# Performance work log

Hardware: AMD Instinct MI355X
Metric: run time of the kernel (lower is better)

The kernel has to match this reference:

```python
import jax, jax.numpy as jnp
import numpy as np
from jax import lax

BETA = 0.9   # membrane decay
THR = 1.0    # firing threshold (soft reset)
K = 10       # number of time bins
# spatial pyramid for original_shape=(100,368) under 4 stride-2 SAME convs
HW = [(50, 184), (25, 92), (13, 46), (7, 23)]
CH = [4, 8, 16, 32]


def conv(x, w, b, stride=1):
    y = lax.conv_general_dilated(x, w, (stride, stride), 'SAME',
                                 dimension_numbers=('NCHW', 'OIHW', 'NCHW'))
    return y + b[None, :, None, None]


def spike(u):
    # heaviside forward, sigmoid straight-through surrogate backward
    s = (u > 0.0).astype(u.dtype)
    sg = jax.nn.sigmoid(4.0 * u)
    return sg + lax.stop_gradient(s - sg)


def setup_inputs() -> dict:
    key = jax.random.key(0)
    ks = jax.random.split(key, 12)
    T, B = 1000, 1
    x = jax.random.normal(ks[0], (T, B, 1, 100, 368), jnp.float32)

    def w(k, o, i, kh=3, kw=3):
        return 0.1 * jax.random.normal(k, (o, i, kh, kw), jnp.float32)

    inp = {'x': x}
    cin = [1] + CH[:3]
    for li in range(4):
        inp['w%d' % (li + 1)] = w(ks[1 + li], CH[li], cin[li])
        inp['b%d' % (li + 1)] = jnp.zeros((CH[li],), jnp.float32)
    sc = [2 * K * c for c in CH]  # skip channels: [80,160,320,640]
    inp['dw4'] = w(ks[5], 64, sc[3]); inp['db4'] = jnp.zeros((64,), jnp.float32)
    inp['dw3'] = w(ks[6], 32, 64 + sc[2]); inp['db3'] = jnp.zeros((32,), jnp.float32)
    inp['dw2'] = w(ks[7], 16, 32 + sc[1]); inp['db2'] = jnp.zeros((16,), jnp.float32)
    inp['dw1'] = w(ks[8], 8, 16 + sc[0]); inp['db1'] = jnp.zeros((8,), jnp.float32)
    inp['wo'] = w(ks[9], 1, 8, 1, 1); inp['bo'] = jnp.zeros((1,), jnp.float32)
    inp['total_steps'] = 1000
    inp['block_size'] = 100
    return inp


def reference(x, w1, b1, w2, b2, w3, b3, w4, b4,
              dw4, db4, dw3, db3, dw2, db2, dw1, db1, wo, bo,
              total_steps, block_size):
    S = total_steps // K  # steps per bin
    B = x.shape[1]
    xb = x.reshape((K, S) + x.shape[1:])  # [K,S,B,C,H,W]
    mems0 = tuple(jnp.zeros((B, CH[i], HW[i][0], HW[i][1]), x.dtype) for i in range(4))
    enc_w = [(w1, b1), (w2, b2), (w3, b3), (w4, b4)]

    def forward_step(x_t, mems):
        new_mems, spk = [], x_t
        for (wi, bi), m in zip(enc_w, mems):
            m = BETA * m + conv(spk, wi, bi, 2)
            spk = spike(m - THR)
            m = m - spk * THR  # soft reset
            new_mems.append(m)
        return tuple(new_mems)

    def step(carry, x_t):
        mems, sums, sqs = carry
        mems = forward_step(x_t, mems)
        sums = tuple(s + m for s, m in zip(sums, mems))
        sqs = tuple(q + m * m for q, m in zip(sqs, mems))
        return (mems, sums, sqs), None

    def bin_fn(mems, x_bin):
        zeros = tuple(jnp.zeros_like(m) for m in mems)
        (mems, sums, sqs), _ = lax.scan(step, (mems, zeros, zeros), x_bin)
        means = tuple(s / S for s in sums)
        stds = tuple(jnp.sqrt(jnp.maximum(q / S - mu * mu, 1e-8))
                     for q, mu in zip(sqs, means))
        return mems, (means, stds)

    _, (means, stds) = lax.scan(bin_fn, mems0, xb)  # each leaf: [K,B,C,H,W]

    def skip(mean, std):
        # torch.cat([mean0,std0,mean1,std1,...], dim=1) channel ordering
        f = jnp.stack([mean, std], axis=1)        # [K,2,B,C,H,W]
        f = jnp.transpose(f, (2, 0, 1, 3, 4, 5))  # [B,K,2,C,H,W]
        b_, k_, t_, c_, h_, w_ = f.shape
        return f.reshape(b_, k_ * t_ * c_, h_, w_)

    skips = [skip(means[i], stds[i]) for i in range(4)]

    def up(t, hw):
        return jax.image.resize(t, (t.shape[0], t.shape[1], hw[0], hw[1]), 'bilinear')

    relu = jax.nn.relu
    d = relu(conv(skips[3], dw4, db4))
    d = relu(conv(jnp.concatenate([up(d, HW[2]), skips[2]], 1), dw3, db3))
    d = relu(conv(jnp.concatenate([up(d, HW[1]), skips[1]], 1), dw2, db2))
    d = relu(conv(jnp.concatenate([up(d, HW[0]), skips[0]], 1), dw1, db1))
    tau_c = conv(up(d, (100, 368)), wo, bo)  # [B,1,100,368]
    return tau_c
```

## Files before the change

### kernel.cpp

```cpp
#include <hip/hip_runtime.h>

#define KBINS  10
#define SBIN   100
#define BETA   0.9f
#define THR    1.0f
#define CDIV(a,b) (((a)+(b)-1)/(b))


__global__ void k_zero16(float4* __restrict__ p, int n16) {
    int i = blockIdx.x * blockDim.x + threadIdx.x;
    if (i < n16) p[i] = make_float4(0.f, 0.f, 0.f, 0.f);
}

__global__ void k_conv1(const float* __restrict__ x,
                        const float* __restrict__ w1,
                        const float* __restrict__ b1,
                        float* __restrict__ c1, int tcount) {
    int n = blockIdx.x * blockDim.x + threadIdx.x;
    if (n >= tcount * 50 * 46) return;
    int wq  = n % 46;
    int tmp = n / 46;
    int h   = tmp % 50;
    int t   = tmp / 50;
    int w0  = wq * 4;

    const float* xt = x + (size_t)t * 36800;
    float rm2 = (h  < 49)  ? 1.f : 0.f;
    float cm8 = (w0 < 180) ? 1.f : 0.f;
    int   r2  = min(2 * h + 2, 99);
    int   cb  = 2 * w0;
    int   c8  = min(cb + 8, 367);

    const float* row0 = xt + (2 * h) * 368 + cb;
    const float* row1 = row0 + 368;
    const float* row2 = xt + r2 * 368 + cb;

    float tap[3][9];
    #pragma unroll
    for (int j = 0; j < 8; j++) {
        tap[0][j] = row0[j];
        tap[1][j] = row1[j];
        tap[2][j] = row2[j] * rm2;
    }
    tap[0][8] = xt[(2 * h) * 368 + c8] * cm8;
    tap[1][8] = xt[(2 * h + 1) * 368 + c8] * cm8;
    tap[2][8] = xt[r2 * 368 + c8] * (rm2 * cm8);

    float* ot = c1 + (size_t)t * 36800 + h * 184 + w0;
    #pragma unroll
    for (int co = 0; co < 4; co++) {
        float b = b1[co];
        float a0 = b, a1 = b, a2 = b, a3 = b;
        #pragma unroll
        for (int r = 0; r < 3; r++) {
            #pragma unroll
            for (int kw = 0; kw < 3; kw++) {
                float wv = w1[co * 9 + r * 3 + kw];
                a0 = fmaf(tap[r][0 + kw], wv, a0);
                a1 = fmaf(tap[r][2 + kw], wv, a1);
                a2 = fmaf(tap[r][4 + kw], wv, a2);
                a3 = fmaf(tap[r][6 + kw], wv, a3);
            }
        }
        *(float4*)(ot + (size_t)co * 9200) = make_float4(a0, a1, a2, a3);
    }
}

__global__ void k_scan(const float* __restrict__ cbuf,
                       unsigned char* __restrict__ spk,
                       float* __restrict__ skip,
                       float* __restrict__ mstate,
                       int C, int HW, int Win, int Wp, int HpWp,
                       int write_spk, int bin0, int nbins, int init) {
    const int PF = 20;
    int CHW = C * HW;
    int p = blockIdx.x * blockDim.x + threadIdx.x;
    if (p >= CHW) return;
    int c  = p / HW;
    int hw = p - c * HW;
    int h  = hw / Win, w = hw - h * Win;

    const size_t tstr = (size_t)C * HpWp;
    unsigned char* sp = spk + (size_t)bin0 * SBIN * tstr
                      + (size_t)c * HpWp + (h + 1) * Wp + (w + 1);

    float m = init ? 0.0f : mstate[p];
    float va[PF], vb[PF];
    #pragma unroll
    for (int j = 0; j < PF; j++) va[j] = cbuf[(size_t)j * CHW + p];

    const int T = nbins * SBIN;
    for (int k = 0; k < nbins; k++) {
        float s = 0.0f, q = 0.0f;
        for (int b = 0; b < SBIN / PF; b++) {
            int t0 = k * SBIN + b * PF;
            int tn = t0 + PF;
            bool more = (tn < T);
            #pragma unroll
            for (int j = 0; j < PF; j++)
                vb[j] = more ? cbuf[(size_t)(tn + j) * CHW + p] : 0.0f;
            #pragma unroll
            for (int j = 0; j < PF; j++) {
                m = fmaf(m, BETA, va[j]);
                float spv = (m - THR > 0.0f) ? 1.0f : 0.0f;
                m -= spv * THR;
                if (write_spk) sp[(size_t)(t0 + j) * tstr] = (unsigned char)spv;
                s += m;
                q = fmaf(m, m, q);
            }
            #pragma unroll
            for (int j = 0; j < PF; j++) va[j] = vb[j];
        }
        int g = bin0 + k;
        float mean = s * (1.0f / SBIN);
        float var  = q * (1.0f / SBIN) - mean * mean;
        float sd   = sqrtf(fmaxf(var, 1e-8f));
        skip[(size_t)(g * 2 * C + c) * HW + hw]     = mean;
        skip[(size_t)(g * 2 * C + C + c) * HW + hw] = sd;
    }
    mstate[p] = m;
}

template<int CIN, int COUT, int COG, int OW,
         int HOUT, int WOUT, int PADH, int HP, int WP>
__global__ void k_convs2(const unsigned char* __restrict__ spk,
                         const float* __restrict__ wt,
                         const float* __restrict__ bias,
                         float* __restrict__ out) {
    const int WQ = (WOUT + OW - 1) / OW;
    const int NT = 2 * OW + 1;
    int n = blockIdx.x * blockDim.x + threadIdx.x;
    if (n >= 1000 * HOUT * WQ) return;
    int wq  = n % WQ;
    int tmp = n / WQ;
    int h   = tmp % HOUT;
    int t   = tmp / HOUT;
    int cog = blockIdx.y;
    int w0  = wq * OW;

    const unsigned char* base = spk + (size_t)t * CIN * HP * WP
                              + (2 * h - PADH + 1) * WP + (2 * w0 + 1);

    float acc[OW][COG];
    #pragma unroll
    for (int q = 0; q < OW; q++)
        #pragma unroll
        for (int co = 0; co < COG; co++) acc[q][co] = bias[cog * COG + co];

    for (int ci = 0; ci < CIN; ci++) {
        const unsigned char* ic = base + (size_t)ci * HP * WP;
        float tap[3][NT];
        #pragma unroll
        for (int r = 0; r < 3; r++)
            #pragma unroll
            for (int j = 0; j < NT; j++)
                tap[r][j] = (float)ic[r * WP + j];
        #pragma unroll
        for (int co = 0; co < COG; co++) {
            const float* wc = wt + ((size_t)(cog * COG + co) * CIN + ci) * 9;
            #pragma unroll
            for (int r = 0; r < 3; r++)
                #pragma unroll
                for (int kw = 0; kw < 3; kw++) {
                    float wv = wc[r * 3 + kw];
                    #pragma unroll
                    for (int q = 0; q < OW; q++)
                        acc[q][co] = fmaf(tap[r][2 * q + kw], wv, acc[q][co]);
                }
        }
    }

    float* ot = out + ((size_t)t * COUT + cog * COG) * (HOUT * WOUT) + h * WOUT + w0;
    #pragma unroll
    for (int co = 0; co < COG; co++) {
        float* oc = ot + (size_t)co * (HOUT * WOUT);
        if constexpr (OW == 4) {
            *(float4*)oc = make_float4(acc[0][co], acc[1][co], acc[2][co], acc[3][co]);
        } else {
            if (w0 + 2 <= WOUT) *(float2*)oc = make_float2(acc[0][co], acc[1][co]);
            else                oc[0] = acc[0][co];
        }
    }
}

__global__ void k_up_cat(const float* __restrict__ up_src, int Cup, int Hi, int Wi,
                         const float* __restrict__ skip, int Cskip,
                         float* __restrict__ out, int Ho, int Wo) {
    int total = (Cup + Cskip) * Ho * Wo;
    int n = blockIdx.x * blockDim.x + threadIdx.x;
    if (n >= total) return;
    int w   = n % Wo;
    int tmp = n / Wo;
    int h   = tmp % Ho;
    int c   = tmp / Ho;
    float v;
    if (c < Cup) {
        float ph = (h + 0.5f) * (float)Hi / (float)Ho - 0.5f;
        float pw = (w + 0.5f) * (float)Wi / (float)Wo - 0.5f;
        float fh = floorf(ph), fw = floorf(pw);
        int h0 = (int)fh, w0 = (int)fw;
        float ah = ph - fh, aw = pw - fw;
        int h0c = min(max(h0, 0), Hi - 1), h1c = min(max(h0 + 1, 0), Hi - 1);
        int w0c = min(max(w0, 0), Wi - 1), w1c = min(max(w0 + 1, 0), Wi - 1);
        const float* sc = up_src + (size_t)c * Hi * Wi;
        float v00 = sc[h0c * Wi + w0c], v01 = sc[h0c * Wi + w1c];
        float v10 = sc[h1c * Wi + w0c], v11 = sc[h1c * Wi + w1c];
        v = (1.0f - ah) * ((1.0f - aw) * v00 + aw * v01)
          + ah * ((1.0f - aw) * v10 + aw * v11);
    } else {
        v = skip[(size_t)(c - Cup) * Ho * Wo + h * Wo + w];
    }
    out[n] = v;
}

template<int CIN, int CS, int COG>
__global__ void k_dconv(const float* __restrict__ in,
                        const float* __restrict__ wt,
                        float* __restrict__ part,
                        int Cout, int H, int W) {
    int HW  = H * W;
    int pix = blockIdx.x * blockDim.x + threadIdx.x;
    if (pix >= HW) return;
    int co0   = blockIdx.y * COG;
    int chunk = blockIdx.z;
    int h = pix / W, w = pix - h * W;

    int off[9]; float msk[9];
    #pragma unroll
    for (int kh = 0; kh < 3; kh++) {
        int r = h + kh - 1;
        bool rok = (r >= 0) && (r < H);
        int rc = rok ? r : 0;
        #pragma unroll
        for (int kw = 0; kw < 3; kw++) {
            int cc = w + kw - 1;
            bool cok = (cc >= 0) && (cc < W);
            int ccc = cok ? cc : 0;
            off[kh * 3 + kw] = rc * W + ccc;
            msk[kh * 3 + kw] = (rok && cok) ? 1.0f : 0.0f;
        }
    }

    const float* ibase = in + (size_t)chunk * CS * HW;
    const float* wbase = wt + ((size_t)co0 * CIN + (size_t)chunk * CS) * 9;

    float acc[COG];
    #pragma unroll
    for (int co = 0; co < COG; co++) acc[co] = 0.0f;

    #pragma unroll 8
    for (int ci = 0; ci < CS; ci++) {
        const float* ic = ibase + (size_t)ci * HW;
        float tap[9];
        #pragma unroll
        for (int j = 0; j < 9; j++)
            tap[j] = msk[j] * ic[off[j]];
        #pragma unroll
        for (int co = 0; co < COG; co++) {
            const float* wc = wbase + ((size_t)co * CIN + ci) * 9;
            #pragma unroll
            for (int j = 0; j < 9; j++)
                acc[co] = fmaf(tap[j], wc[j], acc[co]);
        }
    }

    float* pp = part + ((size_t)chunk * Cout + co0) * HW + pix;
    #pragma unroll
    for (int co = 0; co < COG; co++) pp[(size_t)co * HW] = acc[co];
}

__global__ void k_reduce_relu(const float* __restrict__ part,
                              const float* __restrict__ bias,
                              float* __restrict__ out,
                              int Cout, int HW, int nchunks) {
    int n = blockIdx.x * blockDim.x + threadIdx.x;
    if (n >= Cout * HW) return;
    int co = n / HW;
    float acc = bias[co];
    for (int c = 0; c < nchunks; c++)
        acc += part[(size_t)c * Cout * HW + n];
    out[n] = fmaxf(acc, 0.0f);
}

__global__ void k_final(const float* __restrict__ d1,
                        const float* __restrict__ wo,
                        const float* __restrict__ bo,
                        float* __restrict__ out) {
    int n = blockIdx.x * blockDim.x + threadIdx.x;
    if (n >= 36800) return;
    int w = n % 368, h = n / 368;
    float ph = (h + 0.5f) * 0.5f - 0.5f;
    float pw = (w + 0.5f) * 0.5f - 0.5f;
    float fh = floorf(ph), fw = floorf(pw);
    int h0 = (int)fh, w0 = (int)fw;
    float ah = ph - fh, aw = pw - fw;
    int h0c = min(max(h0, 0), 49),  h1c = min(max(h0 + 1, 0), 49);
    int w0c = min(max(w0, 0), 183), w1c = min(max(w0 + 1, 0), 183);
    float acc = bo[0];
    #pragma unroll
    for (int c = 0; c < 8; c++) {
        const float* sc = d1 + c * 9200;
        float v00 = sc[h0c * 184 + w0c], v01 = sc[h0c * 184 + w1c];
        float v10 = sc[h1c * 184 + w0c], v11 = sc[h1c * 184 + w1c];
        float v = (1.0f - ah) * ((1.0f - aw) * v00 + aw * v01)
                + ah * ((1.0f - aw) * v10 + aw * v11);
        acc = fmaf(wo[c], v, acc);
    }
    out[n] = acc;
}

extern "C" void kernel_launch(void* const* d_in, const int* in_sizes, int n_in,
                              void* d_out, int out_size, void* d_ws, size_t ws_size,
                              hipStream_t stream) {
    (void)in_sizes; (void)n_in; (void)out_size; (void)ws_size;
    const float* x   = (const float*)d_in[0];
    const float* w1  = (const float*)d_in[1];
    const float* b1  = (const float*)d_in[2];
    const float* w2  = (const float*)d_in[3];
    const float* b2  = (const float*)d_in[4];
    const float* w3  = (const float*)d_in[5];
    const float* b3  = (const float*)d_in[6];
    const float* w4  = (const float*)d_in[7];
    const float* b4  = (const float*)d_in[8];
    const float* dw4 = (const float*)d_in[9];
    const float* db4 = (const float*)d_in[10];
    const float* dw3 = (const float*)d_in[11];
    const float* db3 = (const float*)d_in[12];
    const float* dw2 = (const float*)d_in[13];
    const float* db2 = (const float*)d_in[14];
    const float* dw1 = (const float*)d_in[15];
    const float* db1 = (const float*)d_in[16];
    const float* wo  = (const float*)d_in[17];
    const float* bo  = (const float*)d_in[18];
    float* out = (float*)d_out;

    char* ws = (char*)d_ws;
    size_t off = 0;
    auto alloc = [&](size_t bytes) -> void* {
        void* p = ws + off;
        off += (bytes + 255) & ~(size_t)255;
        return p;
    };
    float* cbuf = (float*)alloc(73600000);
    unsigned char* spk1r = (unsigned char*)alloc(39936000 + 256);
    unsigned char* spk2r = (unsigned char*)alloc(21600000 + 256);
    unsigned char* spk3r = (unsigned char*)alloc(12960000 + 256);
    unsigned char* spk1p = spk1r + 63;
    unsigned char* spk2p = spk2r + 63;
    unsigned char* spk3p = spk3r + 63;
    float* skip0 = (float*)alloc(2944000);
    float* skip1 = (float*)alloc(1472000);
    float* skip2 = (float*)alloc(765440);
    float* skip3 = (float*)alloc(412160);
    float* msS   = (float*)alloc(147200);
    char* dec = (char*)cbuf;
    size_t doff = 0;
    auto dalloc = [&](size_t bytes) -> void* {
        void* p = dec + doff;
        doff += (bytes + 255) & ~(size_t)255;
        return p;
    };
    float* d4   = (float*)dalloc(10304u * 4);
    float* d3   = (float*)dalloc(19136u * 4);
    float* d2   = (float*)dalloc(36800u * 4);
    float* d1   = (float*)dalloc(73600u * 4);
    float* cat3 = (float*)dalloc(229632u * 4);
    float* cat2 = (float*)dalloc(441600u * 4);
    float* cat1 = (float*)dalloc(883200u * 4);
    float* part = (float*)dalloc(230400u * 4);

    const int BS  = 256;
    const int SBS = 64;

    {
        size_t nb = (39936000 + 256) + (21600000 + 256) + (12960000 + 256);
        int n16 = (int)(nb / 16);
        k_zero16<<<CDIV(n16, BS), BS, 0, stream>>>((float4*)spk1r, n16);
    }

    for (int q = 0; q < 2; q++) {
        k_conv1<<<CDIV(500 * 50 * 46, BS), BS, 0, stream>>>(
            x + (size_t)q * 500 * 36800, w1, b1, cbuf, 500);
        k_scan<<<CDIV(36800, SBS), SBS, 0, stream>>>(
            cbuf, spk1p, skip0, msS, 4, 9200, 184, 192, 52 * 192,
            1, 5 * q, 5, (q == 0) ? 1 : 0);
    }

    k_convs2<4, 8, 8, 4, 25, 92, 0, 52, 192>
        <<<dim3(CDIV(1000 * 25 * 23, BS), 1), BS, 0, stream>>>(spk1p, w2, b2, cbuf);
    k_scan<<<CDIV(18400, SBS), SBS, 0, stream>>>(cbuf, spk2p, skip1, msS,
                                                 8, 2300, 92, 100, 27 * 100, 1, 0, 10, 1);

    k_convs2<8, 16, 16, 2, 13, 46, 1, 27, 100>
        <<<dim3(CDIV(1000 * 13 * 23, BS), 1), BS, 0, stream>>>(spk2p, w3, b3, cbuf);
    k_scan<<<CDIV(9568, SBS), SBS, 0, stream>>>(cbuf, spk3p, skip2, msS,
                                                16, 598, 46, 54, 15 * 54, 1, 0, 10, 1);

    k_convs2<16, 32, 16, 2, 7, 23, 1, 15, 54>
        <<<dim3(CDIV(1000 * 7 * 12, BS), 2), BS, 0, stream>>>(spk3p, w4, b4, cbuf);
    k_scan<<<CDIV(5152, SBS), SBS, 0, stream>>>(cbuf, spk1p , skip3, msS,
                                                32, 161, 23, 31, 9 * 31, 0, 0, 10, 1);

    {
        dim3 g(CDIV(161, 64), 16, 20);
        k_dconv<640, 32, 4><<<g, 64, 0, stream>>>(skip3, dw4, part, 64, 7, 23);
        k_reduce_relu<<<CDIV(64 * 161, BS), BS, 0, stream>>>(part, db4, d4, 64, 161, 20);
    }
    {
        k_up_cat<<<CDIV(384 * 598, BS), BS, 0, stream>>>(d4, 64, 7, 23,
                                                         skip2, 320, cat3, 13, 46);
        dim3 g(CDIV(598, 64), 8, 12);
        k_dconv<384, 32, 4><<<g, 64, 0, stream>>>(cat3, dw3, part, 32, 13, 46);
        k_reduce_relu<<<CDIV(32 * 598, BS), BS, 0, stream>>>(part, db3, d3, 32, 598, 12);
    }
    {
        k_up_cat<<<CDIV(192 * 2300, BS), BS, 0, stream>>>(d3, 32, 13, 46,
                                                          skip1, 160, cat2, 25, 92);
        dim3 g(CDIV(2300, 128), 4, 6);
        k_dconv<192, 32, 4><<<g, 128, 0, stream>>>(cat2, dw2, part, 16, 25, 92);
        k_reduce_relu<<<CDIV(16 * 2300, BS), BS, 0, stream>>>(part, db2, d2, 16, 2300, 6);
    }
    {
        k_up_cat<<<CDIV(96 * 9200, BS), BS, 0, stream>>>(d2, 16, 25, 92,
                                                         skip0, 80, cat1, 50, 184);
        dim3 g(CDIV(9200, BS), 2, 3);
        k_dconv<96, 32, 4><<<g, BS, 0, stream>>>(cat1, dw1, part, 8, 50, 184);
        k_reduce_relu<<<CDIV(8 * 9200, BS), BS, 0, stream>>>(part, db1, d1, 8, 9200, 3);
    }
    k_final<<<CDIV(36800, BS), BS, 0, stream>>>(d1, wo, bo, out);
}
```

Measured before the change: 837.3 us.

## Fuse all stages into one cooperative persistent kernel with grid syncs

Turns every stage (zeroing, conv1, scans, stride-2 convs, decoder convs, reductions, upsample-concat, final) into a device function run by one cooperative kernel with grid-stride loops and grid-wide barriers between stages. The aim is to remove the cost of launching about 25 separate kernels. In exchange, the grid is capped at 256 or 512 blocks, which limits parallelism in the big stages. The scan stages also expose only a few thousand threads, and the grid-wide syncs add their own overhead. A fallback multi-kernel path is kept for when the cooperative launch fails.

```diff
diff --git a/kernel.cpp b/kernel.cpp
--- a/kernel.cpp
+++ b/kernel.cpp
@@ -1,4 +1,7 @@
 #include <hip/hip_runtime.h>
+#include <hip/hip_cooperative_groups.h>
+
+namespace cg = cooperative_groups;
 
 #define KBINS  10
 #define SBIN   100
@@ -7,332 +10,446 @@
 #define CDIV(a,b) (((a)+(b)-1)/(b))
 
 
-__global__ void k_zero16(float4* __restrict__ p, int n16) {
-    int i = blockIdx.x * blockDim.x + threadIdx.x;
-    if (i < n16) p[i] = make_float4(0.f, 0.f, 0.f, 0.f);
-}
-
-__global__ void k_conv1(const float* __restrict__ x,
-                        const float* __restrict__ w1,
-                        const float* __restrict__ b1,
-                        float* __restrict__ c1, int tcount) {
-    int n = blockIdx.x * blockDim.x + threadIdx.x;
-    if (n >= tcount * 50 * 46) return;
-    int wq  = n % 46;
-    int tmp = n / 46;
-    int h   = tmp % 50;
-    int t   = tmp / 50;
-    int w0  = wq * 4;
-
-    const float* xt = x + (size_t)t * 36800;
-    float rm2 = (h  < 49)  ? 1.f : 0.f;
-    float cm8 = (w0 < 180) ? 1.f : 0.f;
-    int   r2  = min(2 * h + 2, 99);
-    int   cb  = 2 * w0;
-    int   c8  = min(cb + 8, 367);
-
-    const float* row0 = xt + (2 * h) * 368 + cb;
-    const float* row1 = row0 + 368;
-    const float* row2 = xt + r2 * 368 + cb;
-
-    float tap[3][9];
-    #pragma unroll
-    for (int j = 0; j < 8; j++) {
-        tap[0][j] = row0[j];
-        tap[1][j] = row1[j];
-        tap[2][j] = row2[j] * rm2;
-    }
-    tap[0][8] = xt[(2 * h) * 368 + c8] * cm8;
-    tap[1][8] = xt[(2 * h + 1) * 368 + c8] * cm8;
-    tap[2][8] = xt[r2 * 368 + c8] * (rm2 * cm8);
-
-    float* ot = c1 + (size_t)t * 36800 + h * 184 + w0;
-    #pragma unroll
-    for (int co = 0; co < 4; co++) {
-        float b = b1[co];
-        float a0 = b, a1 = b, a2 = b, a3 = b;
-        #pragma unroll
-        for (int r = 0; r < 3; r++) {
-            #pragma unroll
-            for (int kw = 0; kw < 3; kw++) {
-                float wv = w1[co * 9 + r * 3 + kw];
-                a0 = fmaf(tap[r][0 + kw], wv, a0);
-                a1 = fmaf(tap[r][2 + kw], wv, a1);
-                a2 = fmaf(tap[r][4 + kw], wv, a2);
-                a3 = fmaf(tap[r][6 + kw], wv, a3);
+struct MegaParams {
+    const float *x, *w1, *b1, *w2, *b2, *w3, *b3, *w4, *b4;
+    const float *dw4, *db4, *dw3, *db3, *dw2, *db2, *dw1, *db1, *wo, *bo;
+    float* out;
+    float* cbuf;
+    unsigned char *spk1r;
+    unsigned char *spk1p, *spk2p, *spk3p;
+    float *skip0, *skip1, *skip2, *skip3, *msS;
+    float *d4, *d3, *d2, *d1, *cat3, *cat2, *cat1, *part;
+};
+
+
+__device__ inline void st_zero(unsigned char* base, int n16, int tid, int NT) {
+    float4* z = (float4*)base;
+    for (int i = tid; i < n16; i += NT)
+        z[i] = make_float4(0.f, 0.f, 0.f, 0.f);
+}
+
+__device__ inline void st_conv1(const float* x, const float* w1, const float* b1,
+                                float* cbuf, int q, int tid, int NT) {
+    const int N = 500 * 50 * 46;
+    const float* xb = x + (size_t)q * 500 * 36800;
+    for (int n = tid; n < N; n += NT) {
+        int wq  = n % 46;
+        int tmp = n / 46;
+        int h   = tmp % 50;
+        int t   = tmp / 50;
+        int w0  = wq * 4;
+
+        const float* xt = xb + (size_t)t * 36800;
+        float rm2 = (h  < 49)  ? 1.f : 0.f;
+        float cm8 = (w0 < 180) ? 1.f : 0.f;
+        int   r2  = min(2 * h + 2, 99);
+        int   cb  = 2 * w0;
+        int   c8  = min(cb + 8, 367);
+
+        const float* row0 = xt + (2 * h) * 368 + cb;
+        const float* row1 = row0 + 368;
+        const float* row2 = xt + r2 * 368 + cb;
+
+        float tap[3][9];
+        #pragma unroll
+        for (int j = 0; j < 8; j++) {
+            tap[0][j] = row0[j];
+            tap[1][j] = row1[j];
+            tap[2][j] = row2[j] * rm2;
+        }
+        tap[0][8] = xt[(2 * h) * 368 + c8] * cm8;
+        tap[1][8] = xt[(2 * h + 1) * 368 + c8] * cm8;
+        tap[2][8] = xt[r2 * 368 + c8] * (rm2 * cm8);
+
+        float* ot = cbuf + (size_t)t * 36800 + h * 184 + w0;
+        #pragma unroll
+        for (int co = 0; co < 4; co++) {
+            float b = b1[co];
+            float a0 = b, a1 = b, a2 = b, a3 = b;
+            #pragma unroll
+            for (int r = 0; r < 3; r++) {
+                #pragma unroll
+                for (int kw = 0; kw < 3; kw++) {
+                    float wv = w1[co * 9 + r * 3 + kw];
+                    a0 = fmaf(tap[r][0 + kw], wv, a0);
+                    a1 = fmaf(tap[r][2 + kw], wv, a1);
+                    a2 = fmaf(tap[r][4 + kw], wv, a2);
+                    a3 = fmaf(tap[r][6 + kw], wv, a3);
+                }
             }
-        }
-        *(float4*)(ot + (size_t)co * 9200) = make_float4(a0, a1, a2, a3);
-    }
-}
-
-__global__ void k_scan(const float* __restrict__ cbuf,
-                       unsigned char* __restrict__ spk,
-                       float* __restrict__ skip,
-                       float* __restrict__ mstate,
-                       int C, int HW, int Win, int Wp, int HpWp,
-                       int write_spk, int bin0, int nbins, int init) {
+            *(float4*)(ot + (size_t)co * 9200) = make_float4(a0, a1, a2, a3);
+        }
+    }
+}
+
+__device__ inline void st_scan(const float* cbuf, unsigned char* spk,
+                               float* skip, float* mstate,
+                               int C, int HW, int Win, int Wp, int HpWp,
+                               int write_spk, int bin0, int nbins, int init,
+                               int tid, int NT) {
     const int PF = 20;
     int CHW = C * HW;
-    int p = blockIdx.x * blockDim.x + threadIdx.x;
-    if (p >= CHW) return;
-    int c  = p / HW;
-    int hw = p - c * HW;
-    int h  = hw / Win, w = hw - h * Win;
-
-    const size_t tstr = (size_t)C * HpWp;
-    unsigned char* sp = spk + (size_t)bin0 * SBIN * tstr
-                      + (size_t)c * HpWp + (h + 1) * Wp + (w + 1);
-
-    float m = init ? 0.0f : mstate[p];
-    float va[PF], vb[PF];
-    #pragma unroll
-    for (int j = 0; j < PF; j++) va[j] = cbuf[(size_t)j * CHW + p];
-
-    const int T = nbins * SBIN;
-    for (int k = 0; k < nbins; k++) {
-        float s = 0.0f, q = 0.0f;
-        for (int b = 0; b < SBIN / PF; b++) {
-            int t0 = k * SBIN + b * PF;
-            int tn = t0 + PF;
-            bool more = (tn < T);
-            #pragma unroll
-            for (int j = 0; j < PF; j++)
-                vb[j] = more ? cbuf[(size_t)(tn + j) * CHW + p] : 0.0f;
-            #pragma unroll
-            for (int j = 0; j < PF; j++) {
-                m = fmaf(m, BETA, va[j]);
-                float spv = (m - THR > 0.0f) ? 1.0f : 0.0f;
-                m -= spv * THR;
-                if (write_spk) sp[(size_t)(t0 + j) * tstr] = (unsigned char)spv;
-                s += m;
-                q = fmaf(m, m, q);
+    for (int p = tid; p < CHW; p += NT) {
+        int c  = p / HW;
+        int hw = p - c * HW;
+        int h  = hw / Win, w = hw - h * Win;
+
+        const size_t tstr = (size_t)C * HpWp;
+        unsigned char* sp = spk + (size_t)bin0 * SBIN * tstr
+                          + (size_t)c * HpWp + (h + 1) * Wp + (w + 1);
+
+        float m = init ? 0.0f : mstate[p];
+        float va[PF], vb[PF];
+        #pragma unroll
+        for (int j = 0; j < PF; j++) va[j] = cbuf[(size_t)j * CHW + p];
+
+        const int T = nbins * SBIN;
+        for (int k = 0; k < nbins; k++) {
+            float s = 0.0f, q = 0.0f;
+            for (int b = 0; b < SBIN / PF; b++) {
+                int t0 = k * SBIN + b * PF;
+                int tn = t0 + PF;
+                bool more = (tn < T);
+                #pragma unroll
+                for (int j = 0; j < PF; j++)
+                    vb[j] = more ? cbuf[(size_t)(tn + j) * CHW + p] : 0.0f;
+                #pragma unroll
+                for (int j = 0; j < PF; j++) {
+                    m = fmaf(m, BETA, va[j]);
+                    float spv = (m - THR > 0.0f) ? 1.0f : 0.0f;
+                    m -= spv * THR;
+                    if (write_spk) sp[(size_t)(t0 + j) * tstr] = (unsigned char)spv;
+                    s += m;
+                    q = fmaf(m, m, q);
+                }
+                #pragma unroll
+                for (int j = 0; j < PF; j++) va[j] = vb[j];
             }
-            #pragma unroll
-            for (int j = 0; j < PF; j++) va[j] = vb[j];
-        }
-        int g = bin0 + k;
-        float mean = s * (1.0f / SBIN);
-        float var  = q * (1.0f / SBIN) - mean * mean;
-        float sd   = sqrtf(fmaxf(var, 1e-8f));
-        skip[(size_t)(g * 2 * C + c) * HW + hw]     = mean;
-        skip[(size_t)(g * 2 * C + C + c) * HW + hw] = sd;
-    }
-    mstate[p] = m;
+            int g = bin0 + k;
+            float mean = s * (1.0f / SBIN);
+            float var  = q * (1.0f / SBIN) - mean * mean;
+            float sd   = sqrtf(fmaxf(var, 1e-8f));
+            skip[(size_t)(g * 2 * C + c) * HW + hw]     = mean;
+            skip[(size_t)(g * 2 * C + C + c) * HW + hw] = sd;
+        }
+        mstate[p] = m;
+    }
 }
 
 template<int CIN, int COUT, int COG, int OW,
-         int HOUT, int WOUT, int PADH, int HP, int WP>
-__global__ void k_convs2(const unsigned char* __restrict__ spk,
-                         const float* __restrict__ wt,
-                         const float* __restrict__ bias,
-                         float* __restrict__ out) {
-    const int WQ = (WOUT + OW - 1) / OW;
-    const int NT = 2 * OW + 1;
-    int n = blockIdx.x * blockDim.x + threadIdx.x;
-    if (n >= 1000 * HOUT * WQ) return;
-    int wq  = n % WQ;
-    int tmp = n / WQ;
-    int h   = tmp % HOUT;
-    int t   = tmp / HOUT;
-    int cog = blockIdx.y;
-    int w0  = wq * OW;
-
-    const unsigned char* base = spk + (size_t)t * CIN * HP * WP
-                              + (2 * h - PADH + 1) * WP + (2 * w0 + 1);
-
-    float acc[OW][COG];
-    #pragma unroll
-    for (int q = 0; q < OW; q++)
-        #pragma unroll
-        for (int co = 0; co < COG; co++) acc[q][co] = bias[cog * COG + co];
-
-    for (int ci = 0; ci < CIN; ci++) {
-        const unsigned char* ic = base + (size_t)ci * HP * WP;
-        float tap[3][NT];
-        #pragma unroll
-        for (int r = 0; r < 3; r++)
-            #pragma unroll
-            for (int j = 0; j < NT; j++)
-                tap[r][j] = (float)ic[r * WP + j];
-        #pragma unroll
-        for (int co = 0; co < COG; co++) {
-            const float* wc = wt + ((size_t)(cog * COG + co) * CIN + ci) * 9;
+         int HOUT, int WOUT, int PADH, int HP, int WP, int NCOG>
+__device__ inline void st_convs2(const unsigned char* spk, const float* wt,
+                                 const float* bias, float* out,
+                                 int tid, int NT) {
+    const int WQ  = (WOUT + OW - 1) / OW;
+    const int NB  = 1000 * HOUT * WQ;
+    const int NBr = (NB + 63) & ~63;
+    const int NT9 = 2 * OW + 1;
+    for (int i = tid; i < NBr * NCOG; i += NT) {
+        int cog = i / NBr;
+        int n   = i - cog * NBr;
+        bool ok = (n < NB);
+        n = ok ? n : 0;
+        int wq  = n % WQ;
+        int tmp = n / WQ;
+        int h   = tmp % HOUT;
+        int t   = tmp / HOUT;
+        int w0  = wq * OW;
+
+        const unsigned char* base = spk + (size_t)t * CIN * HP * WP
+                                  + (2 * h - PADH + 1) * WP + (2 * w0 + 1);
+
+        float acc[OW][COG];
+        #pragma unroll
+        for (int q = 0; q < OW; q++)
+            #pragma unroll
+            for (int co = 0; co < COG; co++) acc[q][co] = bias[cog * COG + co];
+
+        for (int ci = 0; ci < CIN; ci++) {
+            const unsigned char* ic = base + (size_t)ci * HP * WP;
+            float tap[3][NT9];
             #pragma unroll
             for (int r = 0; r < 3; r++)
                 #pragma unroll
-                for (int kw = 0; kw < 3; kw++) {
-                    float wv = wc[r * 3 + kw];
+                for (int j = 0; j < NT9; j++)
+                    tap[r][j] = (float)ic[r * WP + j];
+            #pragma unroll
+            for (int co = 0; co < COG; co++) {
+                const float* wc = wt + ((size_t)(cog * COG + co) * CIN + ci) * 9;
+                #pragma unroll
+                for (int r = 0; r < 3; r++)
                     #pragma unroll
-                    for (int q = 0; q < OW; q++)
-                        acc[q][co] = fmaf(tap[r][2 * q + kw], wv, acc[q][co]);
+                    for (int kw = 0; kw < 3; kw++) {
+                        float wv = wc[r * 3 + kw];
+                        #pragma unroll
+                        for (int q = 0; q < OW; q++)
+                            acc[q][co] = fmaf(tap[r][2 * q + kw], wv, acc[q][co]);
+                    }
+            }
+        }
+
+        if (ok) {
+            float* ot = out + ((size_t)t * COUT + cog * COG) * (HOUT * WOUT)
+                      + h * WOUT + w0;
+            #pragma unroll
+            for (int co = 0; co < COG; co++) {
+                float* oc = ot + (size_t)co * (HOUT * WOUT);
+                if constexpr (OW == 4) {
+                    *(float4*)oc = make_float4(acc[0][co], acc[1][co],
+                                               acc[2][co], acc[3][co]);
+                } else {
+                    if (w0 + 2 <= WOUT) *(float2*)oc = make_float2(acc[0][co], acc[1][co]);
+                    else                oc[0] = acc[0][co];
                 }
-        }
-    }
-
-    float* ot = out + ((size_t)t * COUT + cog * COG) * (HOUT * WOUT) + h * WOUT + w0;
-    #pragma unroll
-    for (int co = 0; co < COG; co++) {
-        float* oc = ot + (size_t)co * (HOUT * WOUT);
-        if constexpr (OW == 4) {
-            *(float4*)oc = make_float4(acc[0][co], acc[1][co], acc[2][co], acc[3][co]);
+            }
+        }
+    }
+}
+
+__device__ inline void st_upcat(const float* up_src, int Cup, int Hi, int Wi,
+                                const float* skip, int Cskip,
+                                float* out, int Ho, int Wo, int tid, int NT) {
+    int total = (Cup + Cskip) * Ho * Wo;
+    for (int n = tid; n < total; n += NT) {
+        int w   = n % Wo;
+        int tmp = n / Wo;
+        int h   = tmp % Ho;
+        int c   = tmp / Ho;
+        float v;
+        if (c < Cup) {
+            float ph = (h + 0.5f) * (float)Hi / (float)Ho - 0.5f;
+            float pw = (w + 0.5f) * (float)Wi / (float)Wo - 0.5f;
+            float fh = floorf(ph), fw = floorf(pw);
+            int h0 = (int)fh, w0 = (int)fw;
+            float ah = ph - fh, aw = pw - fw;
+            int h0c = min(max(h0, 0), Hi - 1), h1c = min(max(h0 + 1, 0), Hi - 1);
+            int w0c = min(max(w0, 0), Wi - 1), w1c = min(max(w0 + 1, 0), Wi - 1);
+            const float* sc = up_src + (size_t)c * Hi * Wi;
+            float v00 = sc[h0c * Wi + w0c], v01 = sc[h0c * Wi + w1c];
+            float v10 = sc[h1c * Wi + w0c], v11 = sc[h1c * Wi + w1c];
+            v = (1.0f - ah) * ((1.0f - aw) * v00 + aw * v01)
+              + ah * ((1.0f - aw) * v10 + aw * v11);
         } else {
-            if (w0 + 2 <= WOUT) *(float2*)oc = make_float2(acc[0][co], acc[1][co]);
-            else                oc[0] = acc[0][co];
-        }
-    }
-}
-
-__global__ void k_up_cat(const float* __restrict__ up_src, int Cup, int Hi, int Wi,
-                         const float* __restrict__ skip, int Cskip,
-                         float* __restrict__ out, int Ho, int Wo) {
-    int total = (Cup + Cskip) * Ho * Wo;
-    int n = blockIdx.x * blockDim.x + threadIdx.x;
-    if (n >= total) return;
-    int w   = n % Wo;
-    int tmp = n / Wo;
-    int h   = tmp % Ho;
-    int c   = tmp / Ho;
-    float v;
-    if (c < Cup) {
-        float ph = (h + 0.5f) * (float)Hi / (float)Ho - 0.5f;
-        float pw = (w + 0.5f) * (float)Wi / (float)Wo - 0.5f;
+            v = skip[(size_t)(c - Cup) * Ho * Wo + h * Wo + w];
+        }
+        out[n] = v;
+    }
+}
+
+template<int CIN, int CS, int COG>
+__device__ inline void st_dconv(const float* in, const float* wt, float* part,
+                                int Cout, int H, int W, int nchunks,
+                                int tid, int NT) {
+    int HW  = H * W;
+    int HWr = (HW + 63) & ~63;
+    int ncog = Cout / COG;
+    int total = nchunks * ncog * HWr;
+    for (int i = tid; i < total; i += NT) {
+        int pix = i % HWr;
+        int r   = i / HWr;
+        int co0   = (r % ncog) * COG;
+        int chunk = r / ncog;
+        bool ok = (pix < HW);
+        pix = ok ? pix : 0;
+        int h = pix / W, w = pix - h * W;
+
+        int off[9]; float msk[9];
+        #pragma unroll
+        for (int kh = 0; kh < 3; kh++) {
+            int rr = h + kh - 1;
+            bool rok = (rr >= 0) && (rr < H);
+            int rc = rok ? rr : 0;
+            #pragma unroll
+            for (int kw = 0; kw < 3; kw++) {
+                int cc = w + kw - 1;
+                bool cok = (cc >= 0) && (cc < W);
+                int ccc = cok ? cc : 0;
+                off[kh * 3 + kw] = rc * W + ccc;
+                msk[kh * 3 + kw] = (rok && cok) ? 1.0f : 0.0f;
+            }
+        }
+
+        const float* ibase = in + (size_t)chunk * CS * HW;
+        const float* wbase = wt + ((size_t)co0 * CIN + (size_t)chunk * CS) * 9;
+
+        float acc[COG];
+        #pragma unroll
+        for (int co = 0; co < COG; co++) acc[co] = 0.0f;
+
+        #pragma unroll 8
+        for (int ci = 0; ci < CS; ci++) {
+            const float* ic = ibase + (size_t)ci * HW;
+            float tap[9];
+            #pragma unroll
+            for (int j = 0; j < 9; j++)
+                tap[j] = msk[j] * ic[off[j]];
+            #pragma unroll
+            for (int co = 0; co < COG; co++) {
+                const float* wc = wbase + ((size_t)co * CIN + ci) * 9;
+                #pragma unroll
+                for (int j = 0; j < 9; j++)
+                    acc[co] = fmaf(tap[j], wc[j], acc[co]);
+            }
+        }
+
+        if (ok) {
+            float* pp = part + ((size_t)chunk * Cout + co0) * HW + pix;
+            #pragma unroll
+            for (int co = 0; co < COG; co++) pp[(size_t)co * HW] = acc[co];
+        }
+    }
+}
+
+__device__ inline void st_reduce(const float* part, const float* bias,
+                                 float* out, int Cout, int HW, int nchunks,
+                                 int tid, int NT) {
+    int total = Cout * HW;
+    for (int n = tid; n < total; n += NT) {
+        int co = n / HW;
+        float acc = bias[co];
+        for (int c = 0; c < nchunks; c++)
+            acc += part[(size_t)c * Cout * HW + n];
+        out[n] = fmaxf(acc, 0.0f);
+    }
+}
+
+__device__ inline void st_final(const float* d1, const float* wo,
+                                const float* bo, float* out, int tid, int NT) {
+    for (int n = tid; n < 36800; n += NT) {
+        int w = n % 368, h = n / 368;
+        float ph = (h + 0.5f) * 0.5f - 0.5f;
+        float pw = (w + 0.5f) * 0.5f - 0.5f;
         float fh = floorf(ph), fw = floorf(pw);
         int h0 = (int)fh, w0 = (int)fw;
         float ah = ph - fh, aw = pw - fw;
-        int h0c = min(max(h0, 0), Hi - 1), h1c = min(max(h0 + 1, 0), Hi - 1);
-        int w0c = min(max(w0, 0), Wi - 1), w1c = min(max(w0 + 1, 0), Wi - 1);
-        const float* sc = up_src + (size_t)c * Hi * Wi;
-        float v00 = sc[h0c * Wi + w0c], v01 = sc[h0c * Wi + w1c];
-        float v10 = sc[h1c * Wi + w0c], v11 = sc[h1c * Wi + w1c];
-        v = (1.0f - ah) * ((1.0f - aw) * v00 + aw * v01)
-          + ah * ((1.0f - aw) * v10 + aw * v11);
-    } else {
-        v = skip[(size_t)(c - Cup) * Ho * Wo + h * Wo + w];
-    }
-    out[n] = v;
-}
-
+        int h0c = min(max(h0, 0), 49),  h1c = min(max(h0 + 1, 0), 49);
+        int w0c = min(max(w0, 0), 183), w1c = min(max(w0 + 1, 0), 183);
+        float acc = bo[0];
+        #pragma unroll
+        for (int c = 0; c < 8; c++) {
+            const float* sc = d1 + c * 9200;
+            float v00 = sc[h0c * 184 + w0c], v01 = sc[h0c * 184 + w1c];
+            float v10 = sc[h1c * 184 + w0c], v11 = sc[h1c * 184 + w1c];
+            float v = (1.0f - ah) * ((1.0f - aw) * v00 + aw * v01)
+                    + ah * ((1.0f - aw) * v10 + aw * v11);
+            acc = fmaf(wo[c], v, acc);
+        }
+        out[n] = acc;
+    }
+}
+
+__global__ void __launch_bounds__(256, 2) k_mega(MegaParams P) {
+    cg::grid_group grid = cg::this_grid();
+    const int tid = blockIdx.x * 256 + threadIdx.x;
+    const int NT  = gridDim.x * 256;
+
+    st_zero(P.spk1r, 74496768 / 16, tid, NT);
+    grid.sync();
+
+    for (int q = 0; q < 2; q++) {
+        st_conv1(P.x, P.w1, P.b1, P.cbuf, q, tid, NT);
+        grid.sync();
+        st_scan(P.cbuf, P.spk1p, P.skip0, P.msS, 4, 9200, 184, 192, 9984,
+                1, 5 * q, 5, (q == 0) ? 1 : 0, tid, NT);
+        grid.sync();
+    }
+
+    st_convs2<4, 8, 8, 4, 25, 92, 0, 52, 192, 1>(P.spk1p, P.w2, P.b2, P.cbuf, tid, NT);
+    grid.sync();
+    st_scan(P.cbuf, P.spk2p, P.skip1, P.msS, 8, 2300, 92, 100, 2700,
+            1, 0, 10, 1, tid, NT);
+    grid.sync();
+
+    st_convs2<8, 16, 16, 2, 13, 46, 1, 27, 100, 1>(P.spk2p, P.w3, P.b3, P.cbuf, tid, NT);
+    grid.sync();
+    st_scan(P.cbuf, P.spk3p, P.skip2, P.msS, 16, 598, 46, 54, 810,
+            1, 0, 10, 1, tid, NT);
+    grid.sync();
+
+    st_convs2<16, 32, 16, 2, 7, 23, 1, 15, 54, 2>(P.spk3p, P.w4, P.b4, P.cbuf, tid, NT);
+    grid.sync();
+    st_scan(P.cbuf, P.spk1p , P.skip3, P.msS, 32, 161, 23, 31, 279,
+            0, 0, 10, 1, tid, NT);
+    grid.sync();
+
+    st_dconv<640, 32, 4>(P.skip3, P.dw4, P.part, 64, 7, 23, 20, tid, NT);
+    grid.sync();
+    st_reduce(P.part, P.db4, P.d4, 64, 161, 20, tid, NT);
+    grid.sync();
+    st_upcat(P.d4, 64, 7, 23, P.skip2, 320, P.cat3, 13, 46, tid, NT);
+    grid.sync();
+    st_dconv<384, 32, 4>(P.cat3, P.dw3, P.part, 32, 13, 46, 12, tid, NT);
+    grid.sync();
+    st_reduce(P.part, P.db3, P.d3, 32, 598, 12, tid, NT);
+    grid.sync();
+    st_upcat(P.d3, 32, 13, 46, P.skip1, 160, P.cat2, 25, 92, tid, NT);
+    grid.sync();
+    st_dconv<192, 32, 4>(P.cat2, P.dw2, P.part, 16, 25, 92, 6, tid, NT);
+    grid.sync();
+    st_reduce(P.part, P.db2, P.d2, 16, 2300, 6, tid, NT);
+    grid.sync();
+    st_upcat(P.d2, 16, 25, 92, P.skip0, 80, P.cat1, 50, 184, tid, NT);
+    grid.sync();
+    st_dconv<96, 32, 4>(P.cat1, P.dw1, P.part, 8, 50, 184, 3, tid, NT);
+    grid.sync();
+    st_reduce(P.part, P.db1, P.d1, 8, 9200, 3, tid, NT);
+    grid.sync();
+
+    st_final(P.d1, P.wo, P.bo, P.out, tid, NT);
+}
+
+#define TIDNT int tid = blockIdx.x * blockDim.x + threadIdx.x; \
+              int NT = gridDim.x * blockDim.x;
+
+__global__ void g_zero(unsigned char* base, int n16) { TIDNT; st_zero(base, n16, tid, NT); }
+__global__ void g_conv1(const float* x, const float* w1, const float* b1,
+                        float* cbuf, int q) { TIDNT; st_conv1(x, w1, b1, cbuf, q, tid, NT); }
+__global__ void g_scan(const float* cbuf, unsigned char* spk, float* skip,
+                       float* mstate, int C, int HW, int Win, int Wp, int HpWp,
+                       int write_spk, int bin0, int nbins, int init) {
+    TIDNT; st_scan(cbuf, spk, skip, mstate, C, HW, Win, Wp, HpWp,
+                   write_spk, bin0, nbins, init, tid, NT);
+}
+template<int CIN, int COUT, int COG, int OW,
+         int HOUT, int WOUT, int PADH, int HP, int WP, int NCOG>
+__global__ void g_convs2(const unsigned char* spk, const float* wt,
+                         const float* bias, float* out) {
+    TIDNT; st_convs2<CIN, COUT, COG, OW, HOUT, WOUT, PADH, HP, WP, NCOG>(
+        spk, wt, bias, out, tid, NT);
+}
+__global__ void g_upcat(const float* u, int Cup, int Hi, int Wi,
+                        const float* s, int Cs, float* o, int Ho, int Wo) {
+    TIDNT; st_upcat(u, Cup, Hi, Wi, s, Cs, o, Ho, Wo, tid, NT);
+}
 template<int CIN, int CS, int COG>
-__global__ void k_dconv(const float* __restrict__ in,
-                        const float* __restrict__ wt,
-                        float* __restrict__ part,
-                        int Cout, int H, int W) {
-    int HW  = H * W;
-    int pix = blockIdx.x * blockDim.x + threadIdx.x;
-    if (pix >= HW) return;
-    int co0   = blockIdx.y * COG;
-    int chunk = blockIdx.z;
-    int h = pix / W, w = pix - h * W;
-
-    int off[9]; float msk[9];
-    #pragma unroll
-    for (int kh = 0; kh < 3; kh++) {
-        int r = h + kh - 1;
-        bool rok = (r >= 0) && (r < H);
-        int rc = rok ? r : 0;
-        #pragma unroll
-        for (int kw = 0; kw < 3; kw++) {
-            int cc = w + kw - 1;
-            bool cok = (cc >= 0) && (cc < W);
-            int ccc = cok ? cc : 0;
-            off[kh * 3 + kw] = rc * W + ccc;
-            msk[kh * 3 + kw] = (rok && cok) ? 1.0f : 0.0f;
-        }
-    }
-
-    const float* ibase = in + (size_t)chunk * CS * HW;
-    const float* wbase = wt + ((size_t)co0 * CIN + (size_t)chunk * CS) * 9;
-
-    float acc[COG];
-    #pragma unroll
-    for (int co = 0; co < COG; co++) acc[co] = 0.0f;
-
-    #pragma unroll 8
-    for (int ci = 0; ci < CS; ci++) {
-        const float* ic = ibase + (size_t)ci * HW;
-        float tap[9];
-        #pragma unroll
-        for (int j = 0; j < 9; j++)
-            tap[j] = msk[j] * ic[off[j]];
-        #pragma unroll
-        for (int co = 0; co < COG; co++) {
-            const float* wc = wbase + ((size_t)co * CIN + ci) * 9;
-            #pragma unroll
-            for (int j = 0; j < 9; j++)
-                acc[co] = fmaf(tap[j], wc[j], acc[co]);
-        }
-    }
-
-    float* pp = part + ((size_t)chunk * Cout + co0) * HW + pix;
-    #pragma unroll
-    for (int co = 0; co < COG; co++) pp[(size_t)co * HW] = acc[co];
-}
-
-__global__ void k_reduce_relu(const float* __restrict__ part,
-                              const float* __restrict__ bias,
-                              float* __restrict__ out,
-                              int Cout, int HW, int nchunks) {
-    int n = blockIdx.x * blockDim.x + threadIdx.x;
-    if (n >= Cout * HW) return;
-    int co = n / HW;
-    float acc = bias[co];
-    for (int c = 0; c < nchunks; c++)
-        acc += part[(size_t)c * Cout * HW + n];
-    out[n] = fmaxf(acc, 0.0f);
-}
-
-__global__ void k_final(const float* __restrict__ d1,
-                        const float* __restrict__ wo,
-                        const float* __restrict__ bo,
-                        float* __restrict__ out) {
-    int n = blockIdx.x * blockDim.x + threadIdx.x;
-    if (n >= 36800) return;
-    int w = n % 368, h = n / 368;
-    float ph = (h + 0.5f) * 0.5f - 0.5f;
-    float pw = (w + 0.5f) * 0.5f - 0.5f;
-    float fh = floorf(ph), fw = floorf(pw);
-    int h0 = (int)fh, w0 = (int)fw;
-    float ah = ph - fh, aw = pw - fw;
-    int h0c = min(max(h0, 0), 49),  h1c = min(max(h0 + 1, 0), 49);
-    int w0c = min(max(w0, 0), 183), w1c = min(max(w0 + 1, 0), 183);
-    float acc = bo[0];
-    #pragma unroll
-    for (int c = 0; c < 8; c++) {
-        const float* sc = d1 + c * 9200;
-        float v00 = sc[h0c * 184 + w0c], v01 = sc[h0c * 184 + w1c];
-        float v10 = sc[h1c * 184 + w0c], v11 = sc[h1c * 184 + w1c];
-        float v = (1.0f - ah) * ((1.0f - aw) * v00 + aw * v01)
-                + ah * ((1.0f - aw) * v10 + aw * v11);
-        acc = fmaf(wo[c], v, acc);
-    }
-    out[n] = acc;
-}
+__global__ void g_dconv(const float* in, const float* wt, float* part,
+                        int Cout, int H, int W, int nchunks) {
+    TIDNT; st_dconv<CIN, CS, COG>(in, wt, part, Cout, H, W, nchunks, tid, NT);
+}
+__global__ void g_reduce(const float* part, const float* bias, float* out,
+                         int Cout, int HW, int nchunks) {
+    TIDNT; st_reduce(part, bias, out, Cout, HW, nchunks, tid, NT);
+}
+__global__ void g_final(const float* d1, const float* wo, const float* bo,
+                        float* out) { TIDNT; st_final(d1, wo, bo, out, tid, NT); }
 
 extern "C" void kernel_launch(void* const* d_in, const int* in_sizes, int n_in,
                               void* d_out, int out_size, void* d_ws, size_t ws_size,
                               hipStream_t stream) {
     (void)in_sizes; (void)n_in; (void)out_size; (void)ws_size;
-    const float* x   = (const float*)d_in[0];
-    const float* w1  = (const float*)d_in[1];
-    const float* b1  = (const float*)d_in[2];
-    const float* w2  = (const float*)d_in[3];
-    const float* b2  = (const float*)d_in[4];
-    const float* w3  = (const float*)d_in[5];
-    const float* b3  = (const float*)d_in[6];
-    const float* w4  = (const float*)d_in[7];
-    const float* b4  = (const float*)d_in[8];
-    const float* dw4 = (const float*)d_in[9];
-    const float* db4 = (const float*)d_in[10];
-    const float* dw3 = (const float*)d_in[11];
-    const float* db3 = (const float*)d_in[12];
-    const float* dw2 = (const float*)d_in[13];
-    const float* db2 = (const float*)d_in[14];
-    const float* dw1 = (const float*)d_in[15];
-    const float* db1 = (const float*)d_in[16];
-    const float* wo  = (const float*)d_in[17];
-    const float* bo  = (const float*)d_in[18];
-    float* out = (float*)d_out;
+
+    MegaParams P;
+    P.x   = (const float*)d_in[0];
+    P.w1  = (const float*)d_in[1];  P.b1 = (const float*)d_in[2];
+    P.w2  = (const float*)d_in[3];  P.b2 = (const float*)d_in[4];
+    P.w3  = (const float*)d_in[5];  P.b3 = (const float*)d_in[6];
+    P.w4  = (const float*)d_in[7];  P.b4 = (const float*)d_in[8];
+    P.dw4 = (const float*)d_in[9];  P.db4 = (const float*)d_in[10];
+    P.dw3 = (const float*)d_in[11]; P.db3 = (const float*)d_in[12];
+    P.dw2 = (const float*)d_in[13]; P.db2 = (const float*)d_in[14];
+    P.dw1 = (const float*)d_in[15]; P.db1 = (const float*)d_in[16];
+    P.wo  = (const float*)d_in[17]; P.bo  = (const float*)d_in[18];
+    P.out = (float*)d_out;
 
     char* ws = (char*)d_ws;
     size_t off = 0;
@@ -341,91 +458,91 @@
         off += (bytes + 255) & ~(size_t)255;
         return p;
     };
-    float* cbuf = (float*)alloc(73600000);
-    unsigned char* spk1r = (unsigned char*)alloc(39936000 + 256);
+    P.cbuf  = (float*)alloc(73600000);
+    P.spk1r = (unsigned char*)alloc(39936000 + 256);
     unsigned char* spk2r = (unsigned char*)alloc(21600000 + 256);
     unsigned char* spk3r = (unsigned char*)alloc(12960000 + 256);
-    unsigned char* spk1p = spk1r + 63;
-    unsigned char* spk2p = spk2r + 63;
-    unsigned char* spk3p = spk3r + 63;
-    float* skip0 = (float*)alloc(2944000);
-    float* skip1 = (float*)alloc(1472000);
-    float* skip2 = (float*)alloc(765440);
-    float* skip3 = (float*)alloc(412160);
-    float* msS   = (float*)alloc(147200);
-    char* dec = (char*)cbuf;
+    P.spk1p = P.spk1r + 63;
+    P.spk2p = spk2r + 63;
+    P.spk3p = spk3r + 63;
+    P.skip0 = (float*)alloc(2944000);
+    P.skip1 = (float*)alloc(1472000);
+    P.skip2 = (float*)alloc(765440);
+    P.skip3 = (float*)alloc(412160);
+    P.msS   = (float*)alloc(147200);
+    char* dec = (char*)P.cbuf;
     size_t doff = 0;
     auto dalloc = [&](size_t bytes) -> void* {
         void* p = dec + doff;
         doff += (bytes + 255) & ~(size_t)255;
         return p;
     };
-    float* d4   = (float*)dalloc(10304u * 4);
-    float* d3   = (float*)dalloc(19136u * 4);
-    float* d2   = (float*)dalloc(36800u * 4);
-    float* d1   = (float*)dalloc(73600u * 4);
-    float* cat3 = (float*)dalloc(229632u * 4);
-    float* cat2 = (float*)dalloc(441600u * 4);
-    float* cat1 = (float*)dalloc(883200u * 4);
-    float* part = (float*)dalloc(230400u * 4);
-
-    const int BS  = 256;
-    const int SBS = 64;
-
+    P.d4   = (float*)dalloc(10304u * 4);
+    P.d3   = (float*)dalloc(19136u * 4);
+    P.d2   = (float*)dalloc(36800u * 4);
+    P.d1   = (float*)dalloc(73600u * 4);
+    P.cat3 = (float*)dalloc(229632u * 4);
+    P.cat2 = (float*)dalloc(441600u * 4);
+    P.cat1 = (float*)dalloc(883200u * 4);
+    P.part = (float*)dalloc(230400u * 4);
+
+    bool coop_ok = false;
     {
-        size_t nb = (39936000 + 256) + (21600000 + 256) + (12960000 + 256);
-        int n16 = (int)(nb / 16);
-        k_zero16<<<CDIV(n16, BS), BS, 0, stream>>>((float4*)spk1r, n16);
-    }
+        int occ = 0;
+        hipError_t e = hipOccupancyMaxActiveBlocksPerMultiprocessor(
+            &occ, (const void*)k_mega, 256, 0);
+        if (e == hipSuccess && occ >= 1) {
+            int grid = (occ >= 2) ? 512 : 256;
+            void* args[] = { &P };
+            e = hipLaunchCooperativeKernel((const void*)k_mega, dim3(grid),
+                                           dim3(256), args, 0, stream);
+            coop_ok = (e == hipSuccess);
+        }
+    }
+    if (coop_ok) return;
+
+    const int BS = 256, SBS = 64;
+    g_zero<<<CDIV(74496768 / 16, BS), BS, 0, stream>>>(P.spk1r, 74496768 / 16);
 
     for (int q = 0; q < 2; q++) {
-        k_conv1<<<CDIV(500 * 50 * 46, BS), BS, 0, stream>>>(
-            x + (size_t)q * 500 * 36800, w1, b1, cbuf, 500);
-        k_scan<<<CDIV(36800, SBS), SBS, 0, stream>>>(
-            cbuf, spk1p, skip0, msS, 4, 9200, 184, 192, 52 * 192,
+        g_conv1<<<CDIV(500 * 50 * 46, BS), BS, 0, stream>>>(P.x, P.w1, P.b1, P.cbuf, q);
+        g_scan<<<CDIV(36800, SBS), SBS, 0, stream>>>(
+            P.cbuf, P.spk1p, P.skip0, P.msS, 4, 9200, 184, 192, 9984,
             1, 5 * q, 5, (q == 0) ? 1 : 0);
     }
 
-    k_convs2<4, 8, 8, 4, 25, 92, 0, 52, 192>
-        <<<dim3(CDIV(1000 * 25 * 23, BS), 1), BS, 0, stream>>>(spk1p, w2, b2, cbuf);
-    k_scan<<<CDIV(18400, SBS), SBS, 0, stream>>>(cbuf, spk2p, skip1, msS,
-                                                 8, 2300, 92, 100, 27 * 100, 1, 0, 10, 1);
-
-    k_convs2<8, 16, 16, 2, 13, 46, 1, 27, 100>
-        <<<dim3(CDIV(1000 * 13 * 23, BS), 1), BS, 0, stream>>>(spk2p, w3, b3, cbuf);
-    k_scan<<<CDIV(9568, SBS), SBS, 0, stream>>>(cbuf, spk3p, skip2, msS,
-                                                16, 598, 46, 54, 15 * 54, 1, 0, 10, 1);
-
-    k_convs2<16, 32, 16, 2, 7, 23, 1, 15, 54>
-        <<<dim3(CDIV(1000 * 7 * 12, BS), 2), BS, 0, stream>>>(spk3p, w4, b4, cbuf);
-    k_scan<<<CDIV(5152, SBS), SBS, 0, stream>>>(cbuf, spk1p , skip3, msS,
-                                                32, 161, 23, 31, 9 * 31, 0, 0, 10, 1);
-
-    {
-        dim3 g(CDIV(161, 64), 16, 20);
-        k_dconv<640, 32, 4><<<g, 64, 0, stream>>>(skip3, dw4, part, 64, 7, 23);
-        k_reduce_relu<<<CDIV(64 * 161, BS), BS, 0, stream>>>(part, db4, d4, 64, 161, 20);
-    }
-    {
-        k_up_cat<<<CDIV(384 * 598, BS), BS, 0, stream>>>(d4, 64, 7, 23,
-                                                         skip2, 320, cat3, 13, 46);
-        dim3 g(CDIV(598, 64), 8, 12);
-        k_dconv<384, 32, 4><<<g, 64, 0, stream>>>(cat3, dw3, part, 32, 13, 46);
-        k_reduce_relu<<<CDIV(32 * 598, BS), BS, 0, stream>>>(part, db3, d3, 32, 598, 12);
-    }
-    {
-        k_up_cat<<<CDIV(192 * 2300, BS), BS, 0, stream>>>(d3, 32, 13, 46,
-                                                          skip1, 160, cat2, 25, 92);
-        dim3 g(CDIV(2300, 128), 4, 6);
-        k_dconv<192, 32, 4><<<g, 128, 0, stream>>>(cat2, dw2, part, 16, 25, 92);
-        k_reduce_relu<<<CDIV(16 * 2300, BS), BS, 0, stream>>>(part, db2, d2, 16, 2300, 6);
-    }
-    {
-        k_up_cat<<<CDIV(96 * 9200, BS), BS, 0, stream>>>(d2, 16, 25, 92,
-                                                         skip0, 80, cat1, 50, 184);
-        dim3 g(CDIV(9200, BS), 2, 3);
-        k_dconv<96, 32, 4><<<g, BS, 0, stream>>>(cat1, dw1, part, 8, 50, 184);
-        k_reduce_relu<<<CDIV(8 * 9200, BS), BS, 0, stream>>>(part, db1, d1, 8, 9200, 3);
-    }
-    k_final<<<CDIV(36800, BS), BS, 0, stream>>>(d1, wo, bo, out);
-}
+    g_convs2<4, 8, 8, 4, 25, 92, 0, 52, 192, 1>
+        <<<CDIV(575040, BS), BS, 0, stream>>>(P.spk1p, P.w2, P.b2, P.cbuf);
+    g_scan<<<CDIV(18400, SBS), SBS, 0, stream>>>(P.cbuf, P.spk2p, P.skip1, P.msS,
+                                                 8, 2300, 92, 100, 2700, 1, 0, 10, 1);
+
+    g_convs2<8, 16, 16, 2, 13, 46, 1, 27, 100, 1>
+        <<<CDIV(299008, BS), BS, 0, stream>>>(P.spk2p, P.w3, P.b3, P.cbuf);
+    g_scan<<<CDIV(9568, SBS), SBS, 0, stream>>>(P.cbuf, P.spk3p, P.skip2, P.msS,
+                                                16, 598, 46, 54, 810, 1, 0, 10, 1);
+
+    g_convs2<16, 32, 16, 2, 7, 23, 1, 15, 54, 2>
+        <<<CDIV(168064, BS), BS, 0, stream>>>(P.spk3p, P.w4, P.b4, P.cbuf);
+    g_scan<<<CDIV(5152, SBS), SBS, 0, stream>>>(P.cbuf, P.spk1p , P.skip3,
+                                                P.msS, 32, 161, 23, 31, 279, 0, 0, 10, 1);
+
+    g_dconv<640, 32, 4><<<CDIV(20 * 16 * 192, BS), BS, 0, stream>>>(
+        P.skip3, P.dw4, P.part, 64, 7, 23, 20);
+    g_reduce<<<CDIV(64 * 161, BS), BS, 0, stream>>>(P.part, P.db4, P.d4, 64, 161, 20);
+    g_upcat<<<CDIV(384 * 598, BS), BS, 0, stream>>>(P.d4, 64, 7, 23,
+                                                    P.skip2, 320, P.cat3, 13, 46);
+    g_dconv<384, 32, 4><<<CDIV(12 * 8 * 640, BS), BS, 0, stream>>>(
+        P.cat3, P.dw3, P.part, 32, 13, 46, 12);
+    g_reduce<<<CDIV(32 * 598, BS), BS, 0, stream>>>(P.part, P.db3, P.d3, 32, 598, 12);
+    g_upcat<<<CDIV(192 * 2300, BS), BS, 0, stream>>>(P.d3, 32, 13, 46,
+                                                     P.skip1, 160, P.cat2, 25, 92);
+    g_dconv<192, 32, 4><<<CDIV(6 * 4 * 2304, BS), BS, 0, stream>>>(
+        P.cat2, P.dw2, P.part, 16, 25, 92, 6);
+    g_reduce<<<CDIV(16 * 2300, BS), BS, 0, stream>>>(P.part, P.db2, P.d2, 16, 2300, 6);
+    g_upcat<<<CDIV(96 * 9200, BS), BS, 0, stream>>>(P.d2, 16, 25, 92,
+                                                    P.skip0, 80, P.cat1, 50, 184);
+    g_dconv<96, 32, 4><<<CDIV(3 * 2 * 9216, BS), BS, 0, stream>>>(
+        P.cat1, P.dw1, P.part, 8, 50, 184, 3);
+    g_reduce<<<CDIV(8 * 9200, BS), BS, 0, stream>>>(P.part, P.db1, P.d1, 8, 9200, 3);
+    g_final<<<CDIV(36800, BS), BS, 0, stream>>>(P.d1, P.wo, P.bo, P.out);
+}
```

New measurement: 1.572 ms. 1.88x slower.
